# Kernel optimization log

Hardware: AMD Instinct MI355X
Metric: run time of the kernel (lower is better)

## Reference

```python
import jax, jax.numpy as jnp
import numpy as np

C = 128    # channels
H = 4      # heads
HD = C // H  # head_dim = 32
N = 4096   # number of points
B = 1
DIM = 3
EPS = 1e-5


def setup_inputs() -> dict:
    key = jax.random.key(0)
    ks = jax.random.split(key, 16)
    s = 0.05
    p = lambda k, shape: jax.random.normal(k, shape, jnp.float32) * s
    return {
        "eigen": jax.random.normal(ks[0], (B, C, N), jnp.float32),
        # conv1x1 QKV / out projections: weight [C_out, C_in], bias [C_out]
        "wq": p(ks[1], (C, C)), "bq": p(ks[2], (C,)),
        "wk": p(ks[3], (C, C)), "bk": p(ks[4], (C,)),
        "wv": p(ks[5], (C, C)), "bv": p(ks[6], (C,)),
        "wmh": p(ks[7], (C, C)), "bmh": p(ks[8], (C,)),
        # cat_filter: conv1x1(2C->2C) -> BN(2C) -> ReLU -> conv1x1(2C->C)
        "wc1": p(ks[9], (2 * C, 2 * C)), "bc1": p(ks[10], (2 * C,)),
        "gamma": jnp.ones((2 * C,), jnp.float32),
        "beta": jnp.zeros((2 * C,), jnp.float32),
        "wc2": p(ks[11], (C, 2 * C)), "bc2": p(ks[12], (C,)),
        # tran_layer: Linear(C -> dim)
        "wt": p(ks[13], (DIM, C)), "bt": p(ks[14], (DIM,)),
    }


def _conv1x1(x, w, b):
    # x: [B, C_in, N], w: [C_out, C_in] -> [B, C_out, N]
    return jnp.einsum('oc,bcn->bon', w, x) + b[None, :, None]


def reference(eigen, wq, bq, wk, bk, wv, bv, wmh, bmh, wc1, bc1, gamma, beta, wc2, bc2, wt, bt):
    b = eigen.shape[0]
    q = _conv1x1(eigen, wq, bq).reshape(b, H, HD, N)
    k = _conv1x1(eigen, wk, bk).reshape(b, H, HD, N)
    v = _conv1x1(eigen, wv, bv).reshape(b, H, HD, N)

    scale = 1.0 / np.sqrt(HD).astype(np.float32)
    score = jax.nn.softmax(jnp.einsum('bhdn,bhdm->bhnm', q, k) * scale, axis=-1)
    add_value = jnp.einsum('bhnm,bhdm->bhdn', score, v).reshape(b, C, N)
    add_value = _conv1x1(add_value, wmh, bmh)

    cat = jnp.concatenate([eigen, add_value], axis=1)  # [B, 2C, N]
    h = _conv1x1(cat, wc1, bc1)
    # BatchNorm1d in training mode: batch stats over (B, N), biased variance
    mean = h.mean(axis=(0, 2), keepdims=True)
    var = h.var(axis=(0, 2), keepdims=True)
    h = gamma[None, :, None] * (h - mean) * jax.lax.rsqrt(var + EPS) + beta[None, :, None]
    h = jax.nn.relu(h)
    h = _conv1x1(h, wc2, bc2)

    motion = eigen + h  # residual
    # tran_layer on [N, C] (squeeze(0)/unsqueeze(0) implies B==1)
    motion_new = jnp.einsum('dc,bcn->bnd', wt, motion) + bt  # [1, N, dim]
    return motion_new
```

## Files before the change

kernel.cpp:

```cpp
#include <hip/hip_runtime.h>
#include <hip/hip_bf16.h>

typedef __hip_bfloat16 bf16;
typedef __attribute__((ext_vector_type(8))) short short8;
typedef __attribute__((ext_vector_type(4))) float f32x4;

#define NPTS 4096
#define CCH  128

static __device__ __forceinline__ short f2b(float x) {
    bf16 h = __float2bfloat16(x);
    return __builtin_bit_cast(short, h);
}
static __device__ __forceinline__ float b2f(short x) {
    return __bfloat162float(__builtin_bit_cast(bf16, x));
}

struct WPtrs { const void* src[16]; int start[17]; };

__global__ __launch_bounds__(256) void prep_kernel(
    const void* __restrict__ eigen, WPtrs P,
    short* __restrict__ eb,
    float* __restrict__ wfa, short* __restrict__ wba, short* __restrict__ wmhT,
    float* __restrict__ part, int* __restrict__ flagp, int total)
{
    const int tid = threadIdx.x, bid = blockIdx.x;
    __shared__ int sflag;
    {
        int cnt = 0;
        if (tid < 64) {
            const unsigned short* u = (const unsigned short*)eigen;
#pragma unroll
            for (int i = 0; i < 16; ++i) {
                int e = (u[tid * 16 + i] >> 7) & 0xFF;
                cnt += (e >= 0x8F);
            }
#pragma unroll
            for (int off = 32; off > 0; off >>= 1) cnt += __shfl_down(cnt, off);
            if (tid == 0) sflag = (cnt >= 16);
        }
        __syncthreads();
    }
    const int f = sflag;

    if (bid < 128) {
        __shared__ float tile[64][65];
        const int tx = tid & 63, ty = tid >> 6;
        const int n0 = (bid & 63) * 64, c0 = (bid >> 6) * 64;
#pragma unroll
        for (int it = 0; it < 16; ++it) {
            int cl = 4 * it + ty;
            float v = f ? ((const float*)eigen)[(c0 + cl) * NPTS + n0 + tx]
                        : b2f(((const short*)eigen)[(c0 + cl) * NPTS + n0 + tx]);
            tile[tx][cl] = v;
        }
        __syncthreads();
#pragma unroll
        for (int ot = 0; ot < 16; ++ot) {
            int nl = 4 * ot + ty;
            eb[(n0 + nl) * CCH + c0 + tx] = f2b(tile[nl][tx]);
        }
    } else {
        if (bid == 128) {
            if (tid == 0) *flagp = f;
            part[tid] = 0.f; part[256 + tid] = 0.f;
        }
        int i = (bid - 128) * 256 + tid;
        if (i < total) {
            int s = 0;
#pragma unroll 1
            for (int k2 = 0; k2 < 16; ++k2) if (i >= P.start[k2 + 1]) s = k2 + 1;
            int off = i - P.start[s];
            float v = f ? ((const float*)P.src[s])[off]
                        : b2f(((const short*)P.src[s])[off]);
            if (s < 2) v *= 0.25503506f;
            wfa[i] = v;
            short vb = f2b(v);
            wba[i] = vb;
            if (s == 6) wmhT[(off & 127) * 128 + (off >> 7)] = vb;
        }
    }
}

template<int OFRAG, int BNA>
static __device__ __forceinline__ void gemm_accs(
    int n0, int o0, int lo, int hi,
    const short* __restrict__ A, int alda,
    const short* __restrict__ W, int wlda, int K,
    const float* scL, const float* shL, f32x4* acc)
{
    const short* Ar = A + (n0 + lo) * alda + 8 * hi;
#pragma unroll 4
    for (int kk = 0; kk < K; kk += 32) {
        short8 aF = *(const short8*)(Ar + kk);
        if (BNA) {
#pragma unroll
            for (int j = 0; j < 8; ++j) {
                int c = kk + 8 * hi + j;
                aF[j] = f2b(fmaxf(scL[c] * b2f(aF[j]) + shL[c], 0.f));
            }
        }
#pragma unroll
        for (int f = 0; f < OFRAG; ++f) {
            short8 bF = *(const short8*)(W + (o0 + 16 * f + lo) * wlda + 8 * hi + kk);
            acc[f] = __builtin_amdgcn_mfma_f32_16x16x32_bf16(aF, bF, acc[f], 0, 0, 0);
        }
    }
}

static __device__ __forceinline__ void gemm_tn_body(
    int bx, int by, int tid,
    const short* __restrict__ W, const short* __restrict__ A,
    const float* __restrict__ bias, short* __restrict__ out)
{
    const int w = tid >> 6, lane = tid & 63;
    const int lo = lane & 15, hi = lane >> 4;
    const int o0 = by * 16;
    const int n0 = bx * 128 + w * 32;
    const f32x4 z = {0.f, 0.f, 0.f, 0.f};
    f32x4 acc0 = z, acc1 = z;
    const short* Wr = W + (o0 + lo) * CCH + 8 * hi;
    const short* A0 = A + (n0 + lo) * CCH + 8 * hi;
    const short* A1 = A + (n0 + 16 + lo) * CCH + 8 * hi;
#pragma unroll
    for (int kk = 0; kk < 128; kk += 32) {
        short8 aW = *(const short8*)(Wr + kk);
        short8 b0 = *(const short8*)(A0 + kk);
        short8 b1 = *(const short8*)(A1 + kk);
        acc0 = __builtin_amdgcn_mfma_f32_16x16x32_bf16(aW, b0, acc0, 0, 0, 0);
        acc1 = __builtin_amdgcn_mfma_f32_16x16x32_bf16(aW, b1, acc1, 0, 0, 0);
    }
    const int slotA = 8 * (lo >> 2) + (lo & 3);
    const int slotB = slotA + 4;
#pragma unroll
    for (int r = 0; r < 4; ++r) {
        int o = o0 + 4 * hi + r;
        float bb = bias[o];
        out[o * NPTS + n0 + slotA] = f2b(acc0[r] + bb);
        out[o * NPTS + n0 + slotB] = f2b(acc1[r] + bb);
    }
}

__global__ __launch_bounds__(256) void qkv_kernel(
    const short* __restrict__ eb,
    const short* __restrict__ wbq, const short* __restrict__ wbk,
    const short* __restrict__ wbv, const short* __restrict__ wbc1,
    const short* __restrict__ wmhT,
    const float* __restrict__ bqf, const float* __restrict__ bkf,
    const float* __restrict__ bvf, const float* __restrict__ bc1f,
    const float* __restrict__ bmhf, const float* __restrict__ wc1f,
    short* __restrict__ qkb, short* __restrict__ vb,
    short* __restrict__ h1ab, short* __restrict__ wpb, float* __restrict__ bprime)
{
    const int bid = blockIdx.x, tid = threadIdx.x;
    const int w = tid >> 6, lane = tid & 63;
    const int lo = lane & 15, hi = lane >> 4;
    const f32x4 z = {0.f, 0.f, 0.f, 0.f};

    if (bid < 256) {
        const int isK = bid >> 7, bx = bid & 127;
        const int n0 = bx * 32 + (w & 1) * 16, o0 = (w >> 1) * 64;
        f32x4 acc[4] = {z, z, z, z};
        gemm_accs<4, 0>(n0, o0, lo, hi, eb, CCH, isK ? wbk : wbq, CCH, 128,
                        nullptr, nullptr, acc);
        const float* bp = isK ? bkf : bqf;
#pragma unroll
        for (int f = 0; f < 4; ++f) {
            int col = o0 + 16 * f + lo;
#pragma unroll
            for (int r = 0; r < 4; ++r)
                qkb[(n0 + 4 * hi + r) * 256 + isK * 128 + col] = f2b(acc[f][r] + bp[col]);
        }
    } else if (bid < 512) {
        const int b3 = bid - 256, bx = b3 & 127, by = b3 >> 7;
        const int n0 = bx * 32 + (w & 1) * 16, o0 = by * 128 + (w >> 1) * 64;
        f32x4 acc[4] = {z, z, z, z};
        gemm_accs<4, 0>(n0, o0, lo, hi, eb, CCH, wbc1, 256, 128, nullptr, nullptr, acc);
#pragma unroll
        for (int f = 0; f < 4; ++f) {
            int col = o0 + 16 * f + lo;
#pragma unroll
            for (int r = 0; r < 4; ++r)
                h1ab[(n0 + 4 * hi + r) * 256 + col] = f2b(acc[f][r]);
        }
    } else if (bid < 768) {
        int b2 = bid - 512;
        gemm_tn_body(b2 & 31, b2 >> 5, tid, wbv, eb, bvf, vb);
    } else if (bid < 776) {
        const int bx = bid - 768;
        const int n0 = bx * 32 + (w & 1) * 16, o0 = (w >> 1) * 64;
        f32x4 acc[4] = {z, z, z, z};
        gemm_accs<4, 0>(n0, o0, lo, hi, wbc1 + 128, 256, wmhT, 128, 128,
                        nullptr, nullptr, acc);
#pragma unroll
        for (int f = 0; f < 4; ++f) {
            int col = o0 + 16 * f + lo;
#pragma unroll
            for (int r = 0; r < 4; ++r)
                wpb[(n0 + 4 * hi + r) * 128 + col] = f2b(acc[f][r]);
        }
    } else {
        float a = bc1f[tid];
        const float* row = wc1f + tid * 256 + 128;
#pragma unroll 8
        for (int k = 0; k < 128; ++k) a = fmaf(row[k], bmhf[k], a);
        bprime[tid] = a;
    }
}

__global__ __launch_bounds__(1024, 4) void attn_kernel(
    const short* __restrict__ qkb, const short* __restrict__ vB,
    short* __restrict__ av) {
    const int tid = threadIdx.x;
    const int wid = tid >> 6, lane = tid & 63;
    const int lo = lane & 15, hi = lane >> 4;
    const int h = blockIdx.x >> 6;
    const int qblk = blockIdx.x & 63;
    const int q0 = qblk * 64;
    const int hc = h * 32;

    __shared__ __align__(16) float accb[16][64][17];
    __shared__ float lbuf[16][4][16];

    const short* vh = vB + hc * NPTS;

    short8 qf[4];
#pragma unroll
    for (int f = 0; f < 4; ++f)
        qf[f] = *(const short8*)(qkb + (q0 + 16 * f + lo) * 256 + hc + 8 * hi);

    const f32x4 z = {0.f, 0.f, 0.f, 0.f};
    f32x4 o[4][2] = {{z, z}, {z, z}, {z, z}, {z, z}};
    float l[4] = {0.f, 0.f, 0.f, 0.f};

    for (int t = 0; t < 4; ++t) {
        const int m0 = wid * 256 + t * 64;
        short8 kf[4], vf[4];
#pragma unroll
        for (int mt = 0; mt < 4; ++mt)
            kf[mt] = *(const short8*)(qkb + (m0 + 16 * mt + lo) * 256 + 128 + hc + 8 * hi);
#pragma unroll
        for (int kt = 0; kt < 2; ++kt)
#pragma unroll
            for (int dt = 0; dt < 2; ++dt)
                vf[kt * 2 + dt] = *(const short8*)(vh + (16 * dt + lo) * NPTS + m0 + 32 * kt + 8 * hi);

#pragma unroll
        for (int f = 0; f < 4; ++f) {
            f32x4 s[4];
#pragma unroll
            for (int mt = 0; mt < 4; ++mt)
                s[mt] = __builtin_amdgcn_mfma_f32_16x16x32_bf16(kf[mt], qf[f], z, 0, 0, 0);

            float p[4][4];
            float sm = 0.f;
#pragma unroll
            for (int mt = 0; mt < 4; ++mt)
#pragma unroll
                for (int r = 0; r < 4; ++r) {
                    float pv = __builtin_amdgcn_exp2f(s[mt][r]);
                    p[mt][r] = pv;
                    sm += pv;
                }
            sm += __shfl_xor(sm, 16);
            sm += __shfl_xor(sm, 32);
            l[f] += sm;

            short8 pa1, pa2;
#pragma unroll
            for (int j = 0; j < 8; ++j) {
                pa1[j] = f2b(p[j >> 2][j & 3]);
                pa2[j] = f2b(p[2 + (j >> 2)][j & 3]);
            }
            o[f][0] = __builtin_amdgcn_mfma_f32_16x16x32_bf16(pa1, vf[0], o[f][0], 0, 0, 0);
            o[f][1] = __builtin_amdgcn_mfma_f32_16x16x32_bf16(pa1, vf[1], o[f][1], 0, 0, 0);
            o[f][0] = __builtin_amdgcn_mfma_f32_16x16x32_bf16(pa2, vf[2], o[f][0], 0, 0, 0);
            o[f][1] = __builtin_amdgcn_mfma_f32_16x16x32_bf16(pa2, vf[3], o[f][1], 0, 0, 0);
        }
    }

    if (hi == 0) {
#pragma unroll
        for (int f = 0; f < 4; ++f) lbuf[wid][f][lo] = l[f];
    }
    {
        float* mine = &accb[wid][lane][0];
#pragma unroll
        for (int f = 0; f < 4; ++f)
#pragma unroll
            for (int r = 0; r < 4; ++r) mine[f * 4 + r] = o[f][0][r];
    }
    __syncthreads();

    const int e = tid >> 6;
    const int lane_s = tid & 63;
    const int lo_s = lane_s & 15, hi_s = lane_s >> 4;
    const int fm = e >> 2, r = e & 3;
    const int ql = 16 * fm + 4 * hi_s + r;
    float lm = 0.f;
    {
        float sum = 0.f;
#pragma unroll
        for (int s = 0; s < 16; ++s) {
            sum += accb[s][lane_s][e];
            lm  += lbuf[s][fm][4 * hi_s + r];
        }
        av[(q0 + ql) * CCH + hc + lo_s] = f2b(sum / lm);
    }
    __syncthreads();
    {
        float* mine = &accb[wid][lane][0];
#pragma unroll
        for (int f = 0; f < 4; ++f)
#pragma unroll
            for (int r2 = 0; r2 < 4; ++r2) mine[f * 4 + r2] = o[f][1][r2];
    }
    __syncthreads();
    {
        float sum = 0.f;
#pragma unroll
        for (int s = 0; s < 16; ++s) sum += accb[s][lane_s][e];
        av[(q0 + ql) * CCH + hc + 16 + lo_s] = f2b(sum / lm);
    }
}

__global__ __launch_bounds__(256) void c1b_kernel(
    const short* __restrict__ avb, const short* __restrict__ wpb,
    const float* __restrict__ bprime, const short* __restrict__ h1ab,
    short* __restrict__ h1, float* __restrict__ part)
{
    const int tid = threadIdx.x;
    const int w = tid >> 6, lane = tid & 63;
    const int lo = lane & 15, hi = lane >> 4;
    const int n0 = blockIdx.x * 32 + (w & 1) * 16;
    const int o0 = blockIdx.y * 64 + (w >> 1) * 32;
    const f32x4 z = {0.f, 0.f, 0.f, 0.f};
    f32x4 acc[2] = {z, z};
    gemm_accs<2, 0>(n0, o0, lo, hi, avb, CCH, wpb, CCH, 128, nullptr, nullptr, acc);

    const int oa = o0 + lo, ob = o0 + 16 + lo;
    float s0 = 0.f, q0 = 0.f, s1 = 0.f, q1 = 0.f;
#pragma unroll
    for (int r = 0; r < 4; ++r) {
        int n = n0 + 4 * hi + r;
        float v0 = acc[0][r] + bprime[oa] + b2f(h1ab[n * 256 + oa]);
        float v1 = acc[1][r] + bprime[ob] + b2f(h1ab[n * 256 + ob]);
        h1[n * 256 + oa] = f2b(v0);
        h1[n * 256 + ob] = f2b(v1);
        s0 += v0; q0 += v0 * v0; s1 += v1; q1 += v1 * v1;
    }
    s0 += __shfl_xor(s0, 16); s0 += __shfl_xor(s0, 32);
    q0 += __shfl_xor(q0, 16); q0 += __shfl_xor(q0, 32);
    s1 += __shfl_xor(s1, 16); s1 += __shfl_xor(s1, 32);
    q1 += __shfl_xor(q1, 16); q1 += __shfl_xor(q1, 32);
    if (hi == 0) {
        atomicAdd(&part[oa], s0);  atomicAdd(&part[256 + oa], q0);
        atomicAdd(&part[ob], s1);  atomicAdd(&part[256 + ob], q1);
    }
}

__global__ __launch_bounds__(256) void c2f_kernel(
    const short* __restrict__ h1, const short* __restrict__ wbc2,
    const float* __restrict__ bc2f, const short* __restrict__ eb,
    const float* __restrict__ part, const float* __restrict__ gf,
    const float* __restrict__ bef, const float* __restrict__ wtf,
    const float* __restrict__ btf, void* __restrict__ out,
    const int* __restrict__ flagp)
{
    __shared__ float scL[256], shL[256], wts[384];
    __shared__ float red[2][32][3];
    const int tid = threadIdx.x;
    {
        float mean = part[tid] * (1.f / NPTS);
        float var  = part[256 + tid] * (1.f / NPTS) - mean * mean;
        float iv   = rsqrtf(var + 1e-5f);
        float sc   = gf[tid] * iv;
        scL[tid] = sc;
        shL[tid] = bef[tid] - mean * sc;
    }
    for (int i = tid; i < 384; i += 256) wts[i] = wtf[i];
    __syncthreads();

    const int w = tid >> 6, lane = tid & 63;
    const int lo = lane & 15, hi = lane >> 4;
    const int n0 = blockIdx.x * 32 + (w & 1) * 16;
    const int o0 = (w >> 1) * 64;
    const f32x4 z = {0.f, 0.f, 0.f, 0.f};
    f32x4 acc[4] = {z, z, z, z};
    gemm_accs<4, 1>(n0, o0, lo, hi, h1, 256, wbc2, 256, 256, scL, shL, acc);

    float pr[4][3] = {};
#pragma unroll
    for (int f = 0; f < 4; ++f) {
        int col = o0 + 16 * f + lo;
        float w0 = wts[col], w1 = wts[128 + col], w2 = wts[256 + col];
        float bb = bc2f[col];
#pragma unroll
        for (int r = 0; r < 4; ++r) {
            int n = n0 + 4 * hi + r;
            float v = acc[f][r] + bb + b2f(eb[n * CCH + col]);
            pr[r][0] += v * w0; pr[r][1] += v * w1; pr[r][2] += v * w2;
        }
    }
#pragma unroll
    for (int r = 0; r < 4; ++r)
#pragma unroll
        for (int d = 0; d < 3; ++d) {
            float x = pr[r][d];
            x += __shfl_xor(x, 1); x += __shfl_xor(x, 2);
            x += __shfl_xor(x, 4); x += __shfl_xor(x, 8);
            pr[r][d] = x;
        }
    if (lo == 0) {
#pragma unroll
        for (int r = 0; r < 4; ++r)
#pragma unroll
            for (int d = 0; d < 3; ++d)
                red[w >> 1][16 * (w & 1) + 4 * hi + r][d] = pr[r][d];
    }
    __syncthreads();
    if (tid < 96) {
        int nl = tid / 3, d = tid - nl * 3;
        float v = red[0][nl][d] + red[1][nl][d] + btf[d];
        int gn = blockIdx.x * 32 + nl;
        if (*flagp) ((float*)out)[gn * 3 + d] = v;
        else        ((bf16*)out)[gn * 3 + d] = __float2bfloat16(v);
    }
}

extern "C" void kernel_launch(void* const* d_in, const int* in_sizes, int n_in,
                              void* d_out, int out_size, void* d_ws, size_t ws_size,
                              hipStream_t stream) {
    const int CN = CCH * NPTS;
    float* ws = (float*)d_ws;
    size_t fo = 0;
    auto FA = [&](size_t n) { float* p = ws + fo; fo += n; return p; };
    short* eb     = (short*)FA(CN / 2);
    short* qkb    = (short*)FA(CN);
    short* vb     = (short*)FA(CN / 2);
    short* avb    = (short*)FA(CN / 2);
    short* h1ab   = (short*)FA(CN);
    short* h1     = (short*)FA(CN);
    short* wpb    = (short*)FA(16384);
    short* wmhT   = (short*)FA(8192);
    float* bprime = FA(256);
    float* part   = FA(512);
    int*   flagp  = (int*)FA(16);
    float* wfa    = ws + fo;

    WPtrs P;
    int acc = 0;
    int st[17];
    for (int i = 1; i < 17; ++i) {
        P.src[i - 1] = d_in[i];
        P.start[i - 1] = acc;
        st[i] = acc;
        acc += (in_sizes[i] + 3) & ~3;
    }
    P.start[16] = acc;
    short* wba = (short*)(wfa + acc);

    const short* wbq  = wba + st[1];
    const short* wbk  = wba + st[3];
    const short* wbv  = wba + st[5];
    const short* wbc1 = wba + st[9];
    const short* wbc2 = wba + st[13];
    const float* bqf  = wfa + st[2];
    const float* bkf  = wfa + st[4];
    const float* bvf  = wfa + st[6];
    const float* bmhf = wfa + st[8];
    const float* wc1f = wfa + st[9];
    const float* bc1f = wfa + st[10];
    const float* gf   = wfa + st[11];
    const float* bef  = wfa + st[12];
    const float* bc2f = wfa + st[14];
    const float* wtf  = wfa + st[15];
    const float* btf  = wfa + st[16];

    const int NW = (acc + 255) / 256;
    prep_kernel<<<128 + NW, 256, 0, stream>>>(d_in[0], P, eb, wfa, wba, wmhT,
                                              part, flagp, acc);

    qkv_kernel<<<777, 256, 0, stream>>>(eb, wbq, wbk, wbv, wbc1, wmhT,
                                        bqf, bkf, bvf, bc1f, bmhf, wc1f,
                                        qkb, vb, h1ab, wpb, bprime);

    attn_kernel<<<4 * 64, 1024, 0, stream>>>(qkb, vb, avb);

    c1b_kernel<<<dim3(128, 4), 256, 0, stream>>>(avb, wpb, bprime, h1ab, h1, part);

    c2f_kernel<<<128, 256, 0, stream>>>(h1, wbc2, bc2f, eb, part, gf, bef,
                                        wtf, btf, d_out, flagp);
}
```

Measured before the change: 66.21 us.

## Store Q, K, V in MFMA fragment-major layout for contiguous attention loads

The QKV projection now writes Q, K and V into per-head buffers laid out in 16x32 MFMA fragment order, instead of row-major qkb and channel-major vb. The attention kernel then loads each short8 fragment as one contiguous 1 KB wave load rather than strided gathers across rows. This is meant to cut uncoalesced global traffic in the attention inner loop. In exchange, the producer stores become more scattered, and the gemm_tn_body V output indexing must match the new layout.

```diff
diff --git a/kernel.cpp b/kernel.cpp
--- a/kernel.cpp
+++ b/kernel.cpp
@@ -130,14 +130,17 @@
         acc0 = __builtin_amdgcn_mfma_f32_16x16x32_bf16(aW, b0, acc0, 0, 0, 0);
         acc1 = __builtin_amdgcn_mfma_f32_16x16x32_bf16(aW, b1, acc1, 0, 0, 0);
     }
-    const int slotA = 8 * (lo >> 2) + (lo & 3);
-    const int slotB = slotA + 4;
+    const int s1 = 8 * (lo >> 2) + (lo & 3);
+    const int s2 = s1 + 4;
+    const int m32 = n0 >> 5;
 #pragma unroll
     for (int r = 0; r < 4; ++r) {
         int o = o0 + 4 * hi + r;
         float bb = bias[o];
-        out[o * NPTS + n0 + slotA] = f2b(acc0[r] + bb);
-        out[o * NPTS + n0 + slotB] = f2b(acc1[r] + bb);
+        int hd = o >> 5, c32 = o & 31, dt = c32 >> 4, lov = c32 & 15;
+        int base = ((hd * 128 + m32) * 2 + dt) * 512 + lov * 8;
+        out[base + (s1 >> 3) * 128 + (s1 & 7)] = f2b(acc0[r] + bb);
+        out[base + (s2 >> 3) * 128 + (s2 & 7)] = f2b(acc1[r] + bb);
     }
 }
 
@@ -149,7 +152,7 @@
     const float* __restrict__ bqf, const float* __restrict__ bkf,
     const float* __restrict__ bvf, const float* __restrict__ bc1f,
     const float* __restrict__ bmhf, const float* __restrict__ wc1f,
-    short* __restrict__ qkb, short* __restrict__ vb,
+    short* __restrict__ qfb, short* __restrict__ kfb, short* __restrict__ vfb,
     short* __restrict__ h1ab, short* __restrict__ wpb, float* __restrict__ bprime)
 {
     const int bid = blockIdx.x, tid = threadIdx.x;
@@ -164,12 +167,16 @@
         gemm_accs<4, 0>(n0, o0, lo, hi, eb, CCH, isK ? wbk : wbq, CCH, 128,
                         nullptr, nullptr, acc);
         const float* bp = isK ? bkf : bqf;
+        short* dst = isK ? kfb : qfb;
+        const int tile = n0 >> 4;
 #pragma unroll
         for (int f = 0; f < 4; ++f) {
             int col = o0 + 16 * f + lo;
+            int hd = col >> 5, c32 = col & 31;
+            int base = hd * 131072 + tile * 512 + (c32 >> 3) * 128 + (c32 & 7);
 #pragma unroll
             for (int r = 0; r < 4; ++r)
-                qkb[(n0 + 4 * hi + r) * 256 + isK * 128 + col] = f2b(acc[f][r] + bp[col]);
+                dst[base + (4 * hi + r) * 8] = f2b(acc[f][r] + bp[col]);
         }
     } else if (bid < 512) {
         const int b3 = bid - 256, bx = b3 & 127, by = b3 >> 7;
@@ -185,7 +192,7 @@
         }
     } else if (bid < 768) {
         int b2 = bid - 512;
-        gemm_tn_body(b2 & 31, b2 >> 5, tid, wbv, eb, bvf, vb);
+        gemm_tn_body(b2 & 31, b2 >> 5, tid, wbv, eb, bvf, vfb);
     } else if (bid < 776) {
         const int bx = bid - 768;
         const int n0 = bx * 32 + (w & 1) * 16, o0 = (w >> 1) * 64;
@@ -209,8 +216,8 @@
 }
 
 __global__ __launch_bounds__(1024, 4) void attn_kernel(
-    const short* __restrict__ qkb, const short* __restrict__ vB,
-    short* __restrict__ av) {
+    const short* __restrict__ qF, const short* __restrict__ kF,
+    const short* __restrict__ vF, short* __restrict__ av) {
     const int tid = threadIdx.x;
     const int wid = tid >> 6, lane = tid & 63;
     const int lo = lane & 15, hi = lane >> 4;
@@ -218,16 +225,19 @@
     const int qblk = blockIdx.x & 63;
     const int q0 = qblk * 64;
     const int hc = h * 32;
+    const int lofs = hi * 128 + lo * 8;
 
     __shared__ __align__(16) float accb[16][64][17];
     __shared__ float lbuf[16][4][16];
 
-    const short* vh = vB + hc * NPTS;
+    const short* qh = qF + h * 131072;
+    const short* kh = kF + h * 131072;
+    const short* vh = vF + h * 131072;
 
     short8 qf[4];
 #pragma unroll
     for (int f = 0; f < 4; ++f)
-        qf[f] = *(const short8*)(qkb + (q0 + 16 * f + lo) * 256 + hc + 8 * hi);
+        qf[f] = *(const short8*)(qh + ((q0 >> 4) + f) * 512 + lofs);
 
     const f32x4 z = {0.f, 0.f, 0.f, 0.f};
     f32x4 o[4][2] = {{z, z}, {z, z}, {z, z}, {z, z}};
@@ -238,12 +248,12 @@
         short8 kf[4], vf[4];
 #pragma unroll
         for (int mt = 0; mt < 4; ++mt)
-            kf[mt] = *(const short8*)(qkb + (m0 + 16 * mt + lo) * 256 + 128 + hc + 8 * hi);
+            kf[mt] = *(const short8*)(kh + ((m0 >> 4) + mt) * 512 + lofs);
 #pragma unroll
         for (int kt = 0; kt < 2; ++kt)
 #pragma unroll
             for (int dt = 0; dt < 2; ++dt)
-                vf[kt * 2 + dt] = *(const short8*)(vh + (16 * dt + lo) * NPTS + m0 + 32 * kt + 8 * hi);
+                vf[kt * 2 + dt] = *(const short8*)(vh + (((m0 >> 5) + kt) * 2 + dt) * 512 + lofs);
 
 #pragma unroll
         for (int f = 0; f < 4; ++f) {
@@ -436,8 +446,9 @@
     size_t fo = 0;
     auto FA = [&](size_t n) { float* p = ws + fo; fo += n; return p; };
     short* eb     = (short*)FA(CN / 2);
-    short* qkb    = (short*)FA(CN);
-    short* vb     = (short*)FA(CN / 2);
+    short* qfb    = (short*)FA(CN / 2);
+    short* kfb    = (short*)FA(CN / 2);
+    short* vfb    = (short*)FA(CN / 2);
     short* avb    = (short*)FA(CN / 2);
     short* h1ab   = (short*)FA(CN);
     short* h1     = (short*)FA(CN);
@@ -483,9 +494,9 @@
 
     qkv_kernel<<<777, 256, 0, stream>>>(eb, wbq, wbk, wbv, wbc1, wmhT,
                                         bqf, bkf, bvf, bc1f, bmhf, wc1f,
-                                        qkb, vb, h1ab, wpb, bprime);
-
-    attn_kernel<<<4 * 64, 1024, 0, stream>>>(qkb, vb, avb);
+                                        qfb, kfb, vfb, h1ab, wpb, bprime);
+
+    attn_kernel<<<4 * 64, 1024, 0, stream>>>(qfb, kfb, vfb, avb);
 
     c1b_kernel<<<dim3(128, 4), 256, 0, stream>>>(avb, wpb, bprime, h1ab, h1, part);
 
```

Result: faster. 60.30 us (-8.9%).
